# Performance work log

Measured on AMD Instinct MI355X. Metric: run time of the kernel, lower is better.

Reference implementation:

```python
import jax, jax.numpy as jnp
import numpy as np

A0 = 0.5291772105638411
KE = 14.399645351950548
KEHALF = KE / 2.0


def _softplus_inverse(x):
    return float(np.log(np.expm1(x)))


def setup_inputs() -> dict:
    key = jax.random.key(0)
    k_nb, k_mask, k_z, k_r = jax.random.split(key, 4)
    B, A, K = 16, 1024, 1023
    neighbors = jax.random.randint(k_nb, (B, A, K), 0, A)
    neighbor_mask = (jax.random.uniform(k_mask, (B, A, K)) > 0.1).astype(jnp.float32)
    atomic_numbers = jax.random.randint(k_z, (B, A), 1, 95)
    r_ij = jax.random.uniform(k_r, (B, A, K), minval=0.5, maxval=10.0, dtype=jnp.float32)
    p = jnp.float32
    params = {
        "_adiv": jnp.full((1,), _softplus_inverse(1.0 / (0.8854 * A0)), p),
        "_apow": jnp.full((1,), _softplus_inverse(0.23), p),
        "_c1": jnp.full((1,), _softplus_inverse(0.1818), p),
        "_c2": jnp.full((1,), _softplus_inverse(0.5099), p),
        "_c3": jnp.full((1,), _softplus_inverse(0.2802), p),
        "_c4": jnp.full((1,), _softplus_inverse(0.02817), p),
        "_a1": jnp.full((1,), _softplus_inverse(3.2), p),
        "_a2": jnp.full((1,), _softplus_inverse(0.9423), p),
        "_a3": jnp.full((1,), _softplus_inverse(0.4028), p),
        "_a4": jnp.full((1,), _softplus_inverse(0.2016), p),
    }
    return dict(neighbors=neighbors, neighbor_mask=neighbor_mask,
                atomic_numbers=atomic_numbers, r_ij=r_ij, **params)


def reference(neighbors, neighbor_mask, atomic_numbers, r_ij,
              _adiv, _apow, _c1, _c2, _c3, _c4, _a1, _a2, _a3, _a4):
    sp = jax.nn.softplus
    B = neighbors.shape[0]
    Zf = atomic_numbers.astype(jnp.float32)            # [B, A]
    Zp = Zf ** sp(_apow)                               # [B, A] (param [1] broadcasts)
    bidx = jnp.arange(B)[:, None, None]                # batch index for gather
    # gather of symmetric pair quantities without materializing [B, A, A]:
    # a[b,i,j] = Zp[b,i] + Zp[b,j];  zizj[b,i,j] = Zf[b,i] * Zf[b,j]
    Zp_j = Zp[bidx, neighbors]                         # [B, A, K]
    Zf_j = Zf[bidx, neighbors]                         # [B, A, K]
    a = (Zp[:, :, None] + Zp_j) * sp(_adiv) * neighbor_mask
    zizj = Zf[:, :, None] * Zf_j * neighbor_mask
    # normalized mixture coefficients
    c1, c2, c3, c4 = sp(_c1), sp(_c2), sp(_c3), sp(_c4)
    csum = c1 + c2 + c3 + c4
    c1, c2, c3, c4 = c1 / csum, c2 / csum, c3 / csum, c4 / csum
    ar = a * r_ij
    f = (c1 * jnp.exp(-sp(_a1) * ar) + c2 * jnp.exp(-sp(_a2) * ar)
         + c3 * jnp.exp(-sp(_a3) * ar) + c4 * jnp.exp(-sp(_a4) * ar))
    valid = neighbor_mask != 0
    r_safe = jnp.where(valid, r_ij, 1.0)
    corr_ij = jnp.where(valid, KEHALF * f * zizj / r_safe, 0.0)
    return jnp.sum(corr_ij, axis=-1, keepdims=True)    # [B, A, 1]
```

## Files before the change

### kernel.cpp

```cpp
#include <hip/hip_runtime.h>
#include <math.h>

#define KEHALF_F 7.199822675975274f
#define A_ATOMS 1024
#define LOG2E_F 1.4426950408889634f
#define LN2_F   0.6931471805599453f

#if !__has_builtin(__builtin_amdgcn_exp2f)
extern "C" __device__ float __ocml_native_exp2_f32(float);
#endif
#if !__has_builtin(__builtin_amdgcn_logf)
extern "C" __device__ float __ocml_native_log2_f32(float);
#endif

__device__ __forceinline__ float fast_exp2(float x) {
#if __has_builtin(__builtin_amdgcn_exp2f)
    return __builtin_amdgcn_exp2f(x);
#else
    return __ocml_native_exp2_f32(x);
#endif
}
__device__ __forceinline__ float fast_log2(float x) {
#if __has_builtin(__builtin_amdgcn_logf)
    return __builtin_amdgcn_logf(x);
#else
    return __ocml_native_log2_f32(x);
#endif
}
__device__ __forceinline__ float softplus_f(float x) {
    return LN2_F * fast_log2(1.0f + fast_exp2(x * LOG2E_F));
}

__global__ __launch_bounds__(256) void zbl_fused_kernel(
    const int* __restrict__ neighbors,
    const float* __restrict__ neighbor_mask,
    const int* __restrict__ atomic_numbers,
    const float* __restrict__ r_ij,
    const float* __restrict__ p_adiv, const float* __restrict__ p_apow,
    const float* __restrict__ p_c1, const float* __restrict__ p_c2,
    const float* __restrict__ p_c3, const float* __restrict__ p_c4,
    const float* __restrict__ p_a1, const float* __restrict__ p_a2,
    const float* __restrict__ p_a3, const float* __restrict__ p_a4,
    float* __restrict__ out, int K)
{
    __shared__ float2 zz[A_ATOMS];

    const float sp_apow = softplus_f(p_apow[0]);
    const float sp_adiv = softplus_f(p_adiv[0]);
    float c1 = softplus_f(p_c1[0]), c2 = softplus_f(p_c2[0]);
    float c3 = softplus_f(p_c3[0]), c4 = softplus_f(p_c4[0]);
    const float inv_cs = 1.0f / (c1 + c2 + c3 + c4);
    c1 *= inv_cs; c2 *= inv_cs; c3 *= inv_cs; c4 *= inv_cs;
    const float b1 = -softplus_f(p_a1[0]) * LOG2E_F;
    const float b2 = -softplus_f(p_a2[0]) * LOG2E_F;
    const float b3 = -softplus_f(p_a3[0]) * LOG2E_F;
    const float b4 = -softplus_f(p_a4[0]) * LOG2E_F;

    const int row_base = blockIdx.x << 2;
    const int b = row_base >> 10;
    const int* zrow = atomic_numbers + (b << 10);

    for (int t = threadIdx.x; t < A_ATOMS; t += 256) {
        float zf = (float)zrow[t];
        float zp = fast_exp2(sp_apow * fast_log2(zf)) * sp_adiv;
        zz[t] = make_float2(zf, zp);
    }
    __syncthreads();

    const int wid  = threadIdx.x >> 6;
    const int lane = threadIdx.x & 63;
    const int row  = row_base + wid;

    const float2 zi = zz[row & (A_ATOMS - 1)];
    const float zix = KEHALF_F * zi.x;
    const float ziy = zi.y;

    const size_t base = (size_t)row * K;
    const int f = (int)((4 - (int)(base & 3)) & 3);
    const int ngroups = (K - f) >> 2;
    const int tailc   = (K - f) & 3;

    const int*   nb = neighbors     + base;
    const float* mk = neighbor_mask + base;
    const float* rr = r_ij          + base;
    const int4*   nb4 = (const int4*)  (nb + f);
    const float4* mk4 = (const float4*)(mk + f);
    const float4* rr4 = (const float4*)(rr + f);

    float acc = 0.0f;

#define ZBL_TERM(J, M, R)                                                   \
    {                                                                       \
        float2 zj = zz[(J)];                                                \
        float ar = (ziy + zj.y) * (M) * (R);                                \
        float fe = c1 * fast_exp2(b1 * ar) + c2 * fast_exp2(b2 * ar)        \
                 + c3 * fast_exp2(b3 * ar) + c4 * fast_exp2(b4 * ar);       \
        acc += fe * __fdividef(zix * zj.x * (M), (R));                      \
    }

    const int g0 = lane, g1 = lane + 64, g2 = lane + 128, g3 = lane + 192;
    const int g3c   = g3 < ngroups ? g3 : (ngroups - 1);
    const float w3  = g3 < ngroups ? 1.0f : 0.0f;

    int4   j0 = nb4[g0], j1 = nb4[g1], j2 = nb4[g2], j3 = nb4[g3c];
    float4 m0 = mk4[g0], m1 = mk4[g1], m2 = mk4[g2], m3 = mk4[g3c];
    float4 r0 = rr4[g0], r1 = rr4[g1], r2 = rr4[g2], r3 = rr4[g3c];
    m3.x *= w3; m3.y *= w3; m3.z *= w3; m3.w *= w3;

    ZBL_TERM(j0.x, m0.x, r0.x); ZBL_TERM(j0.y, m0.y, r0.y);
    ZBL_TERM(j0.z, m0.z, r0.z); ZBL_TERM(j0.w, m0.w, r0.w);
    ZBL_TERM(j1.x, m1.x, r1.x); ZBL_TERM(j1.y, m1.y, r1.y);
    ZBL_TERM(j1.z, m1.z, r1.z); ZBL_TERM(j1.w, m1.w, r1.w);
    ZBL_TERM(j2.x, m2.x, r2.x); ZBL_TERM(j2.y, m2.y, r2.y);
    ZBL_TERM(j2.z, m2.z, r2.z); ZBL_TERM(j2.w, m2.w, r2.w);
    ZBL_TERM(j3.x, m3.x, r3.x); ZBL_TERM(j3.y, m3.y, r3.y);
    ZBL_TERM(j3.z, m3.z, r3.z); ZBL_TERM(j3.w, m3.w, r3.w);

    int e = -1;
    if (lane < f)                 e = lane;
    else if (lane - f < tailc)    e = f + (ngroups << 2) + (lane - f);
    if (e >= 0) {
        int   j = nb[e];
        float m = mk[e];
        float r = rr[e];
        ZBL_TERM(j, m, r);
    }
#undef ZBL_TERM

    #pragma unroll
    for (int off = 32; off > 0; off >>= 1)
        acc += __shfl_down(acc, off, 64);
    if (lane == 0)
        out[row] = acc;
}

extern "C" void kernel_launch(void* const* d_in, const int* in_sizes, int n_in,
                              void* d_out, int out_size, void* d_ws, size_t ws_size,
                              hipStream_t stream) {
    const int*   neighbors      = (const int*)  d_in[0];
    const float* neighbor_mask  = (const float*)d_in[1];
    const int*   atomic_numbers = (const int*)  d_in[2];
    const float* r_ij           = (const float*)d_in[3];

    float* out = (float*)d_out;

    const int n = in_sizes[2];
    const int K = in_sizes[0] / n;

    zbl_fused_kernel<<<n / 4, 256, 0, stream>>>(
        neighbors, neighbor_mask, atomic_numbers, r_ij,
        (const float*)d_in[4], (const float*)d_in[5],
        (const float*)d_in[6], (const float*)d_in[7],
        (const float*)d_in[8], (const float*)d_in[9],
        (const float*)d_in[10], (const float*)d_in[11],
        (const float*)d_in[12], (const float*)d_in[13],
        out, K);
}
```

Before: 216.2 us.

## Precompute per-atom Z table in a pre-kernel and process 16 rows per block

Moves the per-atom Z^apow computation (log2/exp2 over 1024 atoms) out of every block into a small pre-kernel that writes a float2 table to workspace. The main kernel now uses 512-thread blocks that each handle 16 rows (two passes of 8 waves) and copies the table into shared memory with a single float4 load per thread. This amortizes table setup across four times as many rows per block and removes redundant transcendental work. In exchange it adds a second kernel launch and depends on the workspace being large enough for the table.

```diff
diff --git a/kernel.cpp b/kernel.cpp
--- a/kernel.cpp
+++ b/kernel.cpp
@@ -31,12 +31,25 @@
     return LN2_F * fast_log2(1.0f + fast_exp2(x * LOG2E_F));
 }
 
-__global__ __launch_bounds__(256) void zbl_fused_kernel(
+__global__ __launch_bounds__(256) void zbl_pre_kernel(
+    const int* __restrict__ atomic_numbers,
+    const float* __restrict__ p_adiv, const float* __restrict__ p_apow,
+    float2* __restrict__ tab, int n)
+{
+    const int i = blockIdx.x * 256 + threadIdx.x;
+    if (i < n) {
+        const float sp_apow = softplus_f(p_apow[0]);
+        const float sp_adiv = softplus_f(p_adiv[0]);
+        float zf = (float)atomic_numbers[i];
+        tab[i] = make_float2(zf, fast_exp2(sp_apow * fast_log2(zf)) * sp_adiv);
+    }
+}
+
+__global__ __launch_bounds__(512, 8) void zbl_main_kernel(
     const int* __restrict__ neighbors,
     const float* __restrict__ neighbor_mask,
-    const int* __restrict__ atomic_numbers,
     const float* __restrict__ r_ij,
-    const float* __restrict__ p_adiv, const float* __restrict__ p_apow,
+    const float2* __restrict__ tab,
     const float* __restrict__ p_c1, const float* __restrict__ p_c2,
     const float* __restrict__ p_c3, const float* __restrict__ p_c4,
     const float* __restrict__ p_a1, const float* __restrict__ p_a2,
@@ -45,8 +58,13 @@
 {
     __shared__ float2 zz[A_ATOMS];
 
-    const float sp_apow = softplus_f(p_apow[0]);
-    const float sp_adiv = softplus_f(p_adiv[0]);
+    const int tid = threadIdx.x;
+    const int block_row_base = blockIdx.x << 4;
+    const int b = block_row_base >> 10;
+
+    ((float4*)zz)[tid] = ((const float4*)(tab + ((size_t)b << 10)))[tid];
+    __syncthreads();
+
     float c1 = softplus_f(p_c1[0]), c2 = softplus_f(p_c2[0]);
     float c3 = softplus_f(p_c3[0]), c4 = softplus_f(p_c4[0]);
     const float inv_cs = 1.0f / (c1 + c2 + c3 + c4);
@@ -56,38 +74,8 @@
     const float b3 = -softplus_f(p_a3[0]) * LOG2E_F;
     const float b4 = -softplus_f(p_a4[0]) * LOG2E_F;
 
-    const int row_base = blockIdx.x << 2;
-    const int b = row_base >> 10;
-    const int* zrow = atomic_numbers + (b << 10);
-
-    for (int t = threadIdx.x; t < A_ATOMS; t += 256) {
-        float zf = (float)zrow[t];
-        float zp = fast_exp2(sp_apow * fast_log2(zf)) * sp_adiv;
-        zz[t] = make_float2(zf, zp);
-    }
-    __syncthreads();
-
-    const int wid  = threadIdx.x >> 6;
-    const int lane = threadIdx.x & 63;
-    const int row  = row_base + wid;
-
-    const float2 zi = zz[row & (A_ATOMS - 1)];
-    const float zix = KEHALF_F * zi.x;
-    const float ziy = zi.y;
-
-    const size_t base = (size_t)row * K;
-    const int f = (int)((4 - (int)(base & 3)) & 3);
-    const int ngroups = (K - f) >> 2;
-    const int tailc   = (K - f) & 3;
-
-    const int*   nb = neighbors     + base;
-    const float* mk = neighbor_mask + base;
-    const float* rr = r_ij          + base;
-    const int4*   nb4 = (const int4*)  (nb + f);
-    const float4* mk4 = (const float4*)(mk + f);
-    const float4* rr4 = (const float4*)(rr + f);
-
-    float acc = 0.0f;
+    const int wid  = tid >> 6;
+    const int lane = tid & 63;
 
 #define ZBL_TERM(J, M, R)                                                   \
     {                                                                       \
@@ -98,40 +86,63 @@
         acc += fe * __fdividef(zix * zj.x * (M), (R));                      \
     }
 
-    const int g0 = lane, g1 = lane + 64, g2 = lane + 128, g3 = lane + 192;
-    const int g3c   = g3 < ngroups ? g3 : (ngroups - 1);
-    const float w3  = g3 < ngroups ? 1.0f : 0.0f;
+    #pragma unroll 1
+    for (int p = 0; p < 2; ++p) {
+        const int row = block_row_base + wid + (p << 3);
 
-    int4   j0 = nb4[g0], j1 = nb4[g1], j2 = nb4[g2], j3 = nb4[g3c];
-    float4 m0 = mk4[g0], m1 = mk4[g1], m2 = mk4[g2], m3 = mk4[g3c];
-    float4 r0 = rr4[g0], r1 = rr4[g1], r2 = rr4[g2], r3 = rr4[g3c];
-    m3.x *= w3; m3.y *= w3; m3.z *= w3; m3.w *= w3;
+        const float2 zi = zz[row & (A_ATOMS - 1)];
+        const float zix = KEHALF_F * zi.x;
+        const float ziy = zi.y;
 
-    ZBL_TERM(j0.x, m0.x, r0.x); ZBL_TERM(j0.y, m0.y, r0.y);
-    ZBL_TERM(j0.z, m0.z, r0.z); ZBL_TERM(j0.w, m0.w, r0.w);
-    ZBL_TERM(j1.x, m1.x, r1.x); ZBL_TERM(j1.y, m1.y, r1.y);
-    ZBL_TERM(j1.z, m1.z, r1.z); ZBL_TERM(j1.w, m1.w, r1.w);
-    ZBL_TERM(j2.x, m2.x, r2.x); ZBL_TERM(j2.y, m2.y, r2.y);
-    ZBL_TERM(j2.z, m2.z, r2.z); ZBL_TERM(j2.w, m2.w, r2.w);
-    ZBL_TERM(j3.x, m3.x, r3.x); ZBL_TERM(j3.y, m3.y, r3.y);
-    ZBL_TERM(j3.z, m3.z, r3.z); ZBL_TERM(j3.w, m3.w, r3.w);
+        const size_t base = (size_t)row * K;
+        const int f = (int)((4 - (int)(base & 3)) & 3);
+        const int ngroups = (K - f) >> 2;
+        const int tailc   = (K - f) & 3;
 
-    int e = -1;
-    if (lane < f)                 e = lane;
-    else if (lane - f < tailc)    e = f + (ngroups << 2) + (lane - f);
-    if (e >= 0) {
-        int   j = nb[e];
-        float m = mk[e];
-        float r = rr[e];
-        ZBL_TERM(j, m, r);
+        const int*   nb = neighbors     + base;
+        const float* mk = neighbor_mask + base;
+        const float* rr = r_ij          + base;
+        const int4*   nb4 = (const int4*)  (nb + f);
+        const float4* mk4 = (const float4*)(mk + f);
+        const float4* rr4 = (const float4*)(rr + f);
+
+        float acc = 0.0f;
+
+        const int g0 = lane, g1 = lane + 64, g2 = lane + 128, g3 = lane + 192;
+        const int g3c  = g3 < ngroups ? g3 : (ngroups - 1);
+        const float w3 = g3 < ngroups ? 1.0f : 0.0f;
+
+        int4   j0 = nb4[g0], j1 = nb4[g1], j2 = nb4[g2], j3 = nb4[g3c];
+        float4 m0 = mk4[g0], m1 = mk4[g1], m2 = mk4[g2], m3 = mk4[g3c];
+        float4 r0 = rr4[g0], r1 = rr4[g1], r2 = rr4[g2], r3 = rr4[g3c];
+        m3.x *= w3; m3.y *= w3; m3.z *= w3; m3.w *= w3;
+
+        ZBL_TERM(j0.x, m0.x, r0.x); ZBL_TERM(j0.y, m0.y, r0.y);
+        ZBL_TERM(j0.z, m0.z, r0.z); ZBL_TERM(j0.w, m0.w, r0.w);
+        ZBL_TERM(j1.x, m1.x, r1.x); ZBL_TERM(j1.y, m1.y, r1.y);
+        ZBL_TERM(j1.z, m1.z, r1.z); ZBL_TERM(j1.w, m1.w, r1.w);
+        ZBL_TERM(j2.x, m2.x, r2.x); ZBL_TERM(j2.y, m2.y, r2.y);
+        ZBL_TERM(j2.z, m2.z, r2.z); ZBL_TERM(j2.w, m2.w, r2.w);
+        ZBL_TERM(j3.x, m3.x, r3.x); ZBL_TERM(j3.y, m3.y, r3.y);
+        ZBL_TERM(j3.z, m3.z, r3.z); ZBL_TERM(j3.w, m3.w, r3.w);
+
+        int e = -1;
+        if (lane < f)              e = lane;
+        else if (lane - f < tailc) e = f + (ngroups << 2) + (lane - f);
+        if (e >= 0) {
+            int   j = nb[e];
+            float m = mk[e];
+            float r = rr[e];
+            ZBL_TERM(j, m, r);
+        }
+
+        #pragma unroll
+        for (int off = 32; off > 0; off >>= 1)
+            acc += __shfl_down(acc, off, 64);
+        if (lane == 0)
+            out[row] = acc;
     }
 #undef ZBL_TERM
-
-    #pragma unroll
-    for (int off = 32; off > 0; off >>= 1)
-        acc += __shfl_down(acc, off, 64);
-    if (lane == 0)
-        out[row] = acc;
 }
 
 extern "C" void kernel_launch(void* const* d_in, const int* in_sizes, int n_in,
@@ -142,14 +153,17 @@
     const int*   atomic_numbers = (const int*)  d_in[2];
     const float* r_ij           = (const float*)d_in[3];
 
-    float* out = (float*)d_out;
+    float*  out = (float*)d_out;
+    float2* tab = (float2*)d_ws;
 
     const int n = in_sizes[2];
     const int K = in_sizes[0] / n;
 
-    zbl_fused_kernel<<<n / 4, 256, 0, stream>>>(
-        neighbors, neighbor_mask, atomic_numbers, r_ij,
-        (const float*)d_in[4], (const float*)d_in[5],
+    zbl_pre_kernel<<<(n + 255) / 256, 256, 0, stream>>>(
+        atomic_numbers, (const float*)d_in[4], (const float*)d_in[5], tab, n);
+
+    zbl_main_kernel<<<n / 16, 512, 0, stream>>>(
+        neighbors, neighbor_mask, r_ij, tab,
         (const float*)d_in[6], (const float*)d_in[7],
         (const float*)d_in[8], (const float*)d_in[9],
         (const float*)d_in[10], (const float*)d_in[11],
```

Result: slower. 254.3 us (+17.6%).
